# Kernel tuning notes

Measured on AMD Instinct MI355X. Metric: run time of the kernel, lower is better.

The kernel has to match this reference:

```python
import jax, jax.numpy as jnp
import numpy as np

C = jnp.complex64

def _ry_mat(t):
    c = jnp.cos(t / 2).astype(C)
    s = jnp.sin(t / 2).astype(C)
    return jnp.stack([jnp.stack([c, -s], -1), jnp.stack([s, c], -1)], -2)

def _rx_mat(t):
    c = jnp.cos(t / 2).astype(C)
    s = (-1j) * jnp.sin(t / 2).astype(C)
    return jnp.stack([jnp.stack([c, s], -1), jnp.stack([s, c], -1)], -2)

def _rz_mat(t):
    em = jnp.exp(-1j * (t / 2).astype(C))
    ep = jnp.exp(1j * (t / 2).astype(C))
    z = jnp.zeros_like(em)
    return jnp.stack([jnp.stack([em, z], -1), jnp.stack([z, ep], -1)], -2)

def _apply_1q(psi, gate, w):
    # psi: [bsz, 2^n]; gate: [2,2] (shared) or [bsz,2,2] (per-sample)
    bsz = psi.shape[0]
    s = psi.reshape(bsz, 1 << w, 2, -1)  # wire w isolated on axis 2
    if gate.ndim == 2:
        out = jnp.einsum('ij,bljr->blir', gate, s)
    else:
        out = jnp.einsum('bij,bljr->blir', gate, s)
    return out.reshape(bsz, -1)

def _apply_cnot(psi, c, t):
    bsz = psi.shape[0]
    a, b = min(c, t), max(c, t)
    s = psi.reshape(bsz, 1 << a, 2, 1 << (b - a - 1), 2, -1)
    if c < t:
        # control on axis 2, target on axis 4; after slicing ctrl=1, target -> axis 3
        s = s.at[:, :, 1].set(jnp.flip(s[:, :, 1], axis=3))
    else:
        # control on axis 4, target on axis 2
        s = s.at[:, :, :, :, 1].set(jnp.flip(s[:, :, :, :, 1], axis=2))
    return s.reshape(bsz, -1)

def setup_inputs() -> dict:
    key = jax.random.key(0)
    k1, k2 = jax.random.split(key)
    bsz, n_wires, n_qlayers = 1024, 14, 4
    x_raw = jax.random.normal(k1, (bsz, n_wires), dtype=jnp.float32)
    angles = jax.random.normal(k2, (n_qlayers, n_wires, 3), dtype=jnp.float32) * 0.1
    return {"x_raw": x_raw, "angles": angles}

def reference(x_raw, angles):
    L, n, _ = angles.shape
    bsz = x_raw.shape[0]
    x_enc = jnp.tanh(x_raw[:, :n]) * jnp.pi  # [bsz, n]
    # |0...0> statevector, wire 0 is the most significant bit
    psi = jnp.zeros((bsz, 1 << n), dtype=C).at[:, 0].set(1.0)
    # RY encoding (per-sample angles)
    for w in range(n):
        psi = _apply_1q(psi, _ry_mat(x_enc[:, w]), w)
    # variational layers
    for k in range(L):
        for w in range(n):
            psi = _apply_1q(psi, _rx_mat(angles[k, w, 0]), w)
            psi = _apply_1q(psi, _ry_mat(angles[k, w, 1]), w)
            psi = _apply_1q(psi, _rz_mat(angles[k, w, 2]), w)
        for i in range(n - 1):
            psi = _apply_cnot(psi, i, i + 1)
        psi = _apply_cnot(psi, n - 1, 0)
    # <Z_0>: +|amp|^2 when bit0=0, -|amp|^2 when bit0=1
    p = jnp.abs(psi.reshape(bsz, 2, -1)) ** 2
    return (p[:, 0].sum(-1) - p[:, 1].sum(-1)).astype(jnp.float32)
```

## Files before the change

kernel.cpp:

```cpp
#include <hip/hip_runtime.h>
#include <cmath>
#include <cstdint>

#define NW       14
#define NST      (1 << NW)
#define THREADS  512
#define PRETHR   768
#define NPASS    12
#define WTP      512

typedef _Float16 f16;
typedef _Float16 f16x8 __attribute__((ext_vector_type(8)));
typedef float    f32x4 __attribute__((ext_vector_type(4)));
typedef unsigned short u16;

struct PassArg { u16 Mm[4]; u16 Mt[3]; u16 Mw[3]; };
struct Plan { PassArg ps[NPASS]; u16 initM[14]; u16 measR; u16 _pad; };

__device__ __forceinline__ float2 cmulf(float2 a, float2 b) {
    return make_float2(a.x * b.x - a.y * b.y, a.x * b.y + a.y * b.x);
}
__device__ __host__ __forceinline__ unsigned wtofs(unsigned m, unsigned q01) {
    return (m * 16 + q01 * 8) ^ (((m >> 2) & 1u) << 3);
}

__global__ __launch_bounds__(PRETHR)
void vqc_pre(const float* __restrict__ angles, f16* __restrict__ wt_g,
             float2* __restrict__ u0_g)
{
    __shared__ float2 G[4 * NW * 4];
    const int tid = threadIdx.x;

    if (tid < 4 * NW) {
        const int k = tid / NW, w = tid % NW;
        const float a  = angles[(k * NW + w) * 3 + 0];
        const float bb = angles[(k * NW + w) * 3 + 1];
        const float c  = angles[(k * NW + w) * 3 + 2];
        float sa, ca, sb, cb, sc, cc;
        sincosf(a * 0.5f, &sa, &ca);
        sincosf(bb * 0.5f, &sb, &cb);
        sincosf(c * 0.5f, &sc, &cc);
        float2 m00 = make_float2(cb * ca,  sb * sa);
        float2 m01 = make_float2(-sb * ca, -cb * sa);
        float2 m10 = make_float2(sb * ca,  -cb * sa);
        float2 m11 = make_float2(cb * ca,  -sb * sa);
        const float2 e0 = make_float2(cc, -sc), e1 = make_float2(cc, sc);
        const float2 u00 = cmulf(e0, m00), u01 = cmulf(e0, m01);
        const float2 u10 = cmulf(e1, m10), u11 = cmulf(e1, m11);
        const int gi = (k * NW + w) * 4;
        G[gi + 0] = u00; G[gi + 1] = u01; G[gi + 2] = u10; G[gi + 3] = u11;
        if (k == 0) {
            u0_g[w * 4 + 0] = u00; u0_g[w * 4 + 1] = u01;
            u0_g[w * 4 + 2] = u10; u0_g[w * 4 + 3] = u11;
        }
    }
    __syncthreads();

    {
        const int p = tid >> 6, l6 = tid & 63;
        const int ap = l6 & 15, ahalf = (l6 >> 4) & 1, dup = l6 >> 5;
        const int layer = (p >> 2) + 1, g = p & 3;

        float2 p3;
        if (g == 3) {
            p3 = make_float2((((ap >> 3) & 1) == ahalf) ? 1.f : 0.f, 0.f);
        } else {
            const int wire = 13 - (10 - 4 * g + 3);
            p3 = G[(layer * NW + wire) * 4 + ((ap >> 3) & 1) * 2 + ahalf];
        }
        float2 e0a, e0b, e1a, e1b, e2a, e2b;
        {
            const int r0 = ap & 1, r1 = (ap >> 1) & 1, r2 = (ap >> 2) & 1;
            if (g == 3) {
                const float2* G13 = G + (layer * NW + 13) * 4;
                const float2* G12 = G + (layer * NW + 12) * 4;
                e0a = G13[r0 * 2 + 0]; e0b = G13[r0 * 2 + 1];
                e1a = G12[r1 * 2 + 0]; e1b = G12[r1 * 2 + 1];
                e2a = make_float2(r2 == 0 ? 1.f : 0.f, 0.f);
                e2b = make_float2(r2 == 1 ? 1.f : 0.f, 0.f);
            } else {
                const float2* G0 = G + (layer * NW + (13 - (10 - 4 * g + 0))) * 4;
                const float2* G1 = G + (layer * NW + (13 - (10 - 4 * g + 1))) * 4;
                const float2* G2 = G + (layer * NW + (13 - (10 - 4 * g + 2))) * 4;
                e0a = G0[r0 * 2 + 0]; e0b = G0[r0 * 2 + 1];
                e1a = G1[r1 * 2 + 0]; e1b = G1[r1 * 2 + 1];
                e2a = G2[r2 * 2 + 0]; e2b = G2[r2 * 2 + 1];
            }
        }
        f16x8 frag;
        #pragma unroll
        for (int j2 = 0; j2 < 8; ++j2) {
            float2 v = cmulf(p3, (j2 & 4) ? e2b : e2a);
            v = cmulf(v, (j2 & 2) ? e1b : e1a);
            v = cmulf(v, (j2 & 1) ? e0b : e0a);
            frag[j2] = (f16)(dup ? v.y : v.x);
        }
        *(f16x8*)(wt_g + p * WTP + dup * 256 + wtofs(ap, ahalf)) = frag;
    }
}

__global__ __launch_bounds__(THREADS, 4)
void vqc_kernel(const float* __restrict__ x_raw, const f16* __restrict__ wt_g,
                const float2* __restrict__ u0_g, float* __restrict__ out, Plan pl)
{
    extern __shared__ char smem[];
    f16*    Sh  = (f16*)smem;
    f16*    Wt  = Sh + 2 * NST;
    float2* G0c = (float2*)(Wt + NPASS * WTP);
    float*  red = (float*)(G0c + 2 * NW);

    const int b   = blockIdx.x;
    const int tid = threadIdx.x;
    const int lane = tid & 63, wv = tid >> 6;
    const int q = lane >> 4, m = lane & 15;

    {
        const uint4* src = (const uint4*)wt_g;
        uint4* dst = (uint4*)Wt;
        dst[tid] = src[tid];
        if (tid < 256) dst[512 + tid] = src[512 + tid];
    }
    if (tid < NW) {
        const float xe = tanhf(x_raw[b * NW + tid]) * 3.14159265358979f;
        float se, ce;
        sincosf(xe * 0.5f, &se, &ce);
        const float2 u00 = u0_g[tid * 4 + 0], u01 = u0_g[tid * 4 + 1];
        const float2 u10 = u0_g[tid * 4 + 2], u11 = u0_g[tid * 4 + 3];
        G0c[tid * 2 + 0] = make_float2(u00.x * ce + u01.x * se, u00.y * ce + u01.y * se);
        G0c[tid * 2 + 1] = make_float2(u10.x * ce + u11.x * se, u10.y * ce + u11.y * se);
    }
    __syncthreads();

    {
        float2 common = make_float2(1.f, 0.f);
        #pragma unroll
        for (int bit = 0; bit < 9; ++bit) {
            const int w = 13 - bit;
            const float2 f = ((tid >> bit) & 1) ? G0c[w * 2 + 1] : G0c[w * 2 + 0];
            common = cmulf(common, f);
        }
        unsigned p9 = 0;
        #pragma unroll
        for (int bit = 0; bit < 9; ++bit)
            p9 ^= ((tid >> bit) & 1) ? (unsigned)pl.initM[bit] : 0u;
        float2 f0[2], f1[2], f2[2], f3[2], f4[2];
        f0[0] = G0c[4*2+0]; f0[1] = G0c[4*2+1];
        f1[0] = G0c[3*2+0]; f1[1] = G0c[3*2+1];
        f2[0] = G0c[2*2+0]; f2[1] = G0c[2*2+1];
        f3[0] = G0c[1*2+0]; f3[1] = G0c[1*2+1];
        f4[0] = G0c[0*2+0]; f4[1] = G0c[0*2+1];
        #pragma unroll
        for (int j = 0; j < 32; ++j) {
            float2 o = cmulf(cmulf(f0[j & 1], f1[(j >> 1) & 1]),
                             cmulf(f2[(j >> 2) & 1], f3[(j >> 3) & 1]));
            o = cmulf(o, f4[(j >> 4) & 1]);
            const float2 amp = cmulf(common, o);
            const unsigned ph = p9
                ^ ((j & 1) ? pl.initM[9]  : 0) ^ ((j & 2)  ? pl.initM[10] : 0)
                ^ ((j & 4) ? pl.initM[11] : 0) ^ ((j & 8)  ? pl.initM[12] : 0)
                ^ ((j & 16) ? pl.initM[13] : 0);
            Sh[ph]       = (f16)amp.x;
            Sh[ph + NST] = (f16)amp.y;
        }
    }
    __syncthreads();

    const unsigned plane_off = (unsigned)(q >> 1) << 14;
    const unsigned q01 = (unsigned)(q & 1);
    const f32x4 z4 = {0.f, 0.f, 0.f, 0.f};
    #pragma unroll
    for (int p = 0; p < NPASS; ++p) {
        const PassArg& P = pl.ps[p];
        const unsigned pm = ((m & 1) ? P.Mm[0] : 0) ^ ((m & 2) ? P.Mm[1] : 0)
                          ^ ((m & 4) ? P.Mm[2] : 0) ^ ((m & 8) ? P.Mm[3] : 0);
        const unsigned wb = ((wv & 1) ? P.Mw[0] : 0) ^ ((wv & 2) ? P.Mw[1] : 0)
                          ^ ((wv & 4) ? P.Mw[2] : 0);
        const unsigned b0 = pm ^ wb;
        const f16x8 tr = *(const f16x8*)(Wt + p * WTP +       wtofs((unsigned)m, q01));
        const f16x8 ti = *(const f16x8*)(Wt + p * WTP + 256 + wtofs((unsigned)m, q01));
        const f16x8 bf1 = (q < 2) ? tr : -ti;
        const f16x8 bf2 = (q < 2) ? ti : tr;
        unsigned sw[8];
        f16x8 av[8];
        #pragma unroll
        for (int tt = 0; tt < 8; ++tt) {
            sw[tt] = b0 ^ ((tt & 1) ? P.Mt[0] : 0)
                        ^ ((tt & 2) ? P.Mt[1] : 0)
                        ^ ((tt & 4) ? P.Mt[2] : 0);
            av[tt] = *(const f16x8*)(Sh + plane_off + (sw[tt] ^ (q01 << 3)));
        }
        __syncthreads();
        #pragma unroll
        for (int tt = 0; tt < 8; ++tt) {
            const f32x4 d1 = __builtin_amdgcn_mfma_f32_16x16x32_f16(av[tt], bf1, z4, 0, 0, 0);
            const f32x4 d2 = __builtin_amdgcn_mfma_f32_16x16x32_f16(av[tt], bf2, z4, 0, 0, 0);
            union { f16 h[4]; uint2 u; } c1, c2;
            #pragma unroll
            for (int r = 0; r < 4; ++r) { c1.h[r] = (f16)d1[r]; c2.h[r] = (f16)d2[r]; }
            const unsigned wu = sw[tt] ^ ((unsigned)q << 2);
            *(uint2*)(Sh + wu)       = c1.u;
            *(uint2*)(Sh + NST + wu) = c2.u;
        }
        __syncthreads();
    }

    float acc = 0.f;
    {
        const unsigned base = (unsigned)tid * 32;
        const int pb = __popc(base & (unsigned)pl.measR) & 1;
        #pragma unroll
        for (int cch = 0; cch < 4; ++cch) {
            const unsigned co = (unsigned)cch * 8;
            const f16x8 rr = *(const f16x8*)(Sh + (base ^ co));
            const f16x8 ii = *(const f16x8*)(Sh + NST + (base ^ co));
            #pragma unroll
            for (int e = 0; e < 8; ++e) {
                const float re = (float)rr[e], im = (float)ii[e];
                const float pw = fmaf(re, re, im * im);
                const int sgn = pb ^ (__popc((co | (unsigned)e) & (unsigned)pl.measR) & 1);
                acc += sgn ? -pw : pw;
            }
        }
    }
    #pragma unroll
    for (int off = 32; off > 0; off >>= 1) acc += __shfl_down(acc, off);
    if ((tid & 63) == 0) red[wv] = acc;
    __syncthreads();
    if (tid == 0) {
        float s = 0.f;
        #pragma unroll
        for (int i = 0; i < THREADS / 64; ++i) s += red[i];
        out[b] = s;
    }
}

struct GFm { u16 col[14]; };

static unsigned ringp_host(unsigned x) {
    unsigned s = x;
    s ^= s >> 1; s ^= s >> 2; s ^= s >> 4; s ^= s >> 8;
    s &= 0x3FFFu;
    return (s ^ ((s & 1u) << 13)) & 0x3FFFu;
}
static u16 gf_apply(const GFm& m, u16 v) {
    u16 r = 0;
    for (int b = 0; b < 14; ++b) if ((v >> b) & 1) r ^= m.col[b];
    return r;
}
static GFm gf_compose(const GFm& A, const GFm& B) {
    GFm C;
    for (int b = 0; b < 14; ++b) C.col[b] = gf_apply(A, B.col[b]);
    return C;
}
static void rows_from(const GFm& A, u16 r[14]) {
    for (int i = 0; i < 14; ++i) {
        u16 mm = 0;
        for (int b = 0; b < 14; ++b) mm |= (u16)(((A.col[b] >> i) & 1) << b);
        r[i] = mm;
    }
}
static GFm from_rows(const u16 r[14]) {
    GFm A;
    for (int b = 0; b < 14; ++b) {
        u16 c = 0;
        for (int i = 0; i < 14; ++i) c |= (u16)(((r[i] >> b) & 1) << i);
        A.col[b] = c;
    }
    return A;
}
static GFm gf_inv(const GFm& A) {
    u16 M[14], I[14];
    rows_from(A, M);
    for (int i = 0; i < 14; ++i) I[i] = (u16)(1u << i);
    for (int c = 0; c < 14; ++c) {
        int p = c;
        while (p < 14 && !((M[p] >> c) & 1)) ++p;
        if (p == 14) continue;
        u16 t = M[c]; M[c] = M[p]; M[p] = t;
        t = I[c]; I[c] = I[p]; I[p] = t;
        for (int r2 = 0; r2 < 14; ++r2)
            if (r2 != c && ((M[r2] >> c) & 1)) { M[r2] ^= M[c]; I[r2] ^= I[c]; }
    }
    return from_rows(I);
}

static void build_plan(Plan& pl) {
    GFm ring, ringInv;
    for (int b = 0; b < 14; ++b) ring.col[b] = (u16)ringp_host(1u << b);
    ringInv = gf_inv(ring);

    GFm phi;
    for (int j = 0; j < 4; ++j) phi.col[10 + j] = (u16)(1u << j);
    for (int j = 0; j < 4; ++j) phi.col[6 + j]  = (u16)(1u << (4 + j));
    for (int j = 0; j < 4; ++j) phi.col[2 + j]  = (u16)(1u << (8 + j));
    phi.col[0] = (u16)(1u << 12);
    phi.col[1] = (u16)(1u << 13);

    for (int b = 0; b < 14; ++b) pl.initM[b] = gf_apply(phi, ring.col[b]);

    const int gb[4][4] = {{10,11,12,13},{6,7,8,9},{2,3,4,5},{0,1,6,7}};

    for (int p = 0; p < NPASS; ++p) {
        const int g = p & 3;
        u16 uv[4];
        if (g < 3) for (int j = 0; j < 4; ++j) uv[j] = (u16)(1u << gb[g + 1][j]);
        else       for (int j = 0; j < 4; ++j) uv[j] = ringInv.col[10 + j];
        for (int j = 0; j < 4; ++j) pl.ps[p].Mm[j] = gf_apply(phi, uv[j]);

        u16 span[14]; int ns = 0;
        u16 tv[6]; int nt = 0;
        auto tryAdd = [&](u16 v) -> bool {
            bool ch = true;
            while (ch) {
                ch = false;
                for (int i = 0; i < ns; ++i) {
                    const int tb = 31 - __builtin_clz((unsigned)span[i]);
                    if ((v >> tb) & 1) { v ^= span[i]; ch = true; }
                }
            }
            if (!v) return false;
            span[ns++] = v;
            return true;
        };
        for (int j = 0; j < 4; ++j) tryAdd((u16)(1u << gb[g][j]));
        for (int j = 0; j < 4; ++j) tryAdd(uv[j]);
        for (int b2 = 0; b2 < 14 && nt < 6; ++b2)
            if (tryAdd((u16)(1u << b2))) tv[nt++] = (u16)(1u << b2);
        for (int i = 0; i < 3; ++i) pl.ps[p].Mt[i] = gf_apply(phi, tv[i]);
        for (int i = 0; i < 3; ++i) pl.ps[p].Mw[i] = gf_apply(phi, tv[i + 3]);

        GFm Bm;
        for (int j = 0; j < 4; ++j) Bm.col[j]     = (u16)(1u << gb[g][j]);
        for (int j = 0; j < 4; ++j) Bm.col[4 + j] = uv[j];
        for (int i = 0; i < 6; ++i) Bm.col[8 + i] = tv[i];
        GFm Binv = gf_inv(Bm);
        u16 img[14];
        for (int j = 0; j < 4; ++j) img[j]     = pl.ps[p].Mm[j];
        for (int j = 0; j < 4; ++j) img[4 + j] = (u16)(1u << j);
        for (int i = 0; i < 6; ++i) img[8 + i] = gf_apply(phi, tv[i]);
        GFm nphi;
        for (int b2 = 0; b2 < 14; ++b2) {
            const u16 coef = gf_apply(Binv, (u16)(1u << b2));
            u16 v = 0;
            for (int j = 0; j < 14; ++j) if ((coef >> j) & 1) v ^= img[j];
            nphi.col[b2] = v;
        }
        if (g == 3) nphi = gf_compose(nphi, ringInv);
        phi = nphi;
    }

    GFm pinv = gf_inv(phi);
    u16 rows[14];
    rows_from(pinv, rows);
    pl.measR = rows[13];
    pl._pad = 0;
}

static u16 swz_h(u16 v) {
    return (u16)(v ^ ((((v >> 6) ^ (v >> 9) ^ (v >> 11)) & 7u) << 3));
}
static u16 swzT_h(u16 r) {
    u16 o = r;
    if ((r >> 3) & 1) o ^= (u16)((1u << 6) | (1u << 9)  | (1u << 11));
    if ((r >> 4) & 1) o ^= (u16)((1u << 7) | (1u << 10) | (1u << 12));
    if ((r >> 5) & 1) o ^= (u16)((1u << 8) | (1u << 11) | (1u << 13));
    return o;
}
static void fold_swzu(Plan& pl) {
    for (int p = 0; p < NPASS; ++p) {
        for (int j = 0; j < 4; ++j) pl.ps[p].Mm[j] = swz_h(pl.ps[p].Mm[j]);
        for (int j = 0; j < 3; ++j) pl.ps[p].Mt[j] = swz_h(pl.ps[p].Mt[j]);
        for (int j = 0; j < 3; ++j) pl.ps[p].Mw[j] = swz_h(pl.ps[p].Mw[j]);
    }
    for (int b = 0; b < 14; ++b) pl.initM[b] = swz_h(pl.initM[b]);
    pl.measR = swzT_h(pl.measR);
}

extern "C" void kernel_launch(void* const* d_in, const int* in_sizes, int n_in,
                              void* d_out, int out_size, void* d_ws, size_t ws_size,
                              hipStream_t stream) {
    const float* x_raw  = (const float*)d_in[0];
    const float* angles = (const float*)d_in[1];
    float* out = (float*)d_out;
    const int bsz = in_sizes[0] / NW;

    Plan pl;
    build_plan(pl);
    fold_swzu(pl);

    f16*    wt_g = (f16*)d_ws;
    float2* u0_g = (float2*)((char*)d_ws + (size_t)NPASS * WTP * sizeof(f16));

    vqc_pre<<<dim3(1), dim3(PRETHR), 0, stream>>>(angles, wt_g, u0_g);

    const size_t lds = (size_t)2 * NST * sizeof(f16)
                     + (size_t)NPASS * WTP * sizeof(f16)
                     + (size_t)(2 * NW) * sizeof(float2)
                     + (size_t)(THREADS / 64) * sizeof(float);
    (void)hipFuncSetAttribute((const void*)vqc_kernel,
                              hipFuncAttributeMaxDynamicSharedMemorySize, (int)lds);
    vqc_kernel<<<dim3(bsz), dim3(THREADS), lds, stream>>>(x_raw, wt_g, u0_g, out, pl);
}
```

Baseline: 111.5 us.

## Drop per-pass barrier, vectorize initial state writes, and linearize measurement reads

Removes the __syncthreads between the shared-memory loads and the in-place MFMA writes in each of the 12 passes. This relies on each wave reading and writing only its own addresses, so it saves a block-wide barrier per pass but races if that assumption fails. The product-state initialization is restructured as a shared product tree: each thread emits two 16-element runs as packed f16x8 stores instead of 32 scattered scalar stores. The final <Z0> reduction now reads contiguous, tid-strided chunks with parity computed per address, which should reduce LDS bank conflicts.

```diff
diff --git a/kernel.cpp b/kernel.cpp
--- a/kernel.cpp
+++ b/kernel.cpp
@@ -143,24 +143,59 @@
         #pragma unroll
         for (int bit = 0; bit < 9; ++bit)
             p9 ^= ((tid >> bit) & 1) ? (unsigned)pl.initM[bit] : 0u;
-        float2 f0[2], f1[2], f2[2], f3[2], f4[2];
-        f0[0] = G0c[4*2+0]; f0[1] = G0c[4*2+1];
-        f1[0] = G0c[3*2+0]; f1[1] = G0c[3*2+1];
-        f2[0] = G0c[2*2+0]; f2[1] = G0c[2*2+1];
-        f3[0] = G0c[1*2+0]; f3[1] = G0c[1*2+1];
-        f4[0] = G0c[0*2+0]; f4[1] = G0c[0*2+1];
-        #pragma unroll
-        for (int j = 0; j < 32; ++j) {
-            float2 o = cmulf(cmulf(f0[j & 1], f1[(j >> 1) & 1]),
-                             cmulf(f2[(j >> 2) & 1], f3[(j >> 3) & 1]));
-            o = cmulf(o, f4[(j >> 4) & 1]);
-            const float2 amp = cmulf(common, o);
-            const unsigned ph = p9
-                ^ ((j & 1) ? pl.initM[9]  : 0) ^ ((j & 2)  ? pl.initM[10] : 0)
-                ^ ((j & 4) ? pl.initM[11] : 0) ^ ((j & 8)  ? pl.initM[12] : 0)
-                ^ ((j & 16) ? pl.initM[13] : 0);
-            Sh[ph]       = (f16)amp.x;
-            Sh[ph + NST] = (f16)amp.y;
+
+        const float2 f0a = G0c[4*2+0], f0b = G0c[4*2+1];
+        const float2 f1a = G0c[3*2+0], f1b = G0c[3*2+1];
+        const float2 f2a = G0c[2*2+0], f2b = G0c[2*2+1];
+        const float2 f3a = G0c[1*2+0], f3b = G0c[1*2+1];
+        const float2 f4a = G0c[0*2+0], f4b = G0c[0*2+1];
+
+        const unsigned S   = (unsigned)pl.initM[13];
+        const unsigned Slo = S & 15u, Hh = S & ~15u;
+        const unsigned plo = p9 & 15u, B0 = p9 & ~15u;
+
+        #pragma unroll
+        for (int c = 0; c < 2; ++c) {
+            const unsigned r = plo ^ (c ? Slo : 0u);
+            const bool s0 = ((r       ) & 1u) != 0;
+            const bool s1 = (((r) ^ (r >> 1)) & 1u) != 0;
+            const bool s2 = (((r >> 1) ^ (r >> 2)) & 1u) != 0;
+            const bool s3 = (((r >> 2) ^ (r >> 3)) & 1u) != 0;
+            const bool s4 = ((((r >> 3) & 1u) ^ (unsigned)c) != 0);
+            const float2 F0[2] = { s0 ? f0b : f0a, s0 ? f0a : f0b };
+            const float2 F1[2] = { s1 ? f1b : f1a, s1 ? f1a : f1b };
+            const float2 F2[2] = { s2 ? f2b : f2a, s2 ? f2a : f2b };
+            const float2 F3[2] = { s3 ? f3b : f3a, s3 ? f3a : f3b };
+            const float2 F4[2] = { s4 ? f4b : f4a, s4 ? f4a : f4b };
+            const float2 A0 = cmulf(common, F4[0]);
+            const float2 A1 = cmulf(common, F4[1]);
+            float2 Bt[4];
+            Bt[0] = cmulf(A0, F3[0]); Bt[1] = cmulf(A0, F3[1]);
+            Bt[2] = cmulf(A1, F3[1]); Bt[3] = cmulf(A1, F3[0]);
+            float2 Ct[8];
+            #pragma unroll
+            for (int o32 = 0; o32 < 4; ++o32) {
+                const int o2 = o32 & 1;
+                Ct[o32 * 2 + 0] = cmulf(Bt[o32], F2[o2]);
+                Ct[o32 * 2 + 1] = cmulf(Bt[o32], F2[1 ^ o2]);
+            }
+            float2 Gt[4];
+            Gt[0] = cmulf(F1[0], F0[0]); Gt[1] = cmulf(F1[1], F0[1]);
+            Gt[2] = cmulf(F1[1], F0[0]); Gt[3] = cmulf(F1[0], F0[1]);
+
+            union { f16 h[8]; f16x8 v; } hR[2], hI[2];
+            #pragma unroll
+            for (int o = 0; o < 16; ++o) {
+                const int o0 = o & 1, o1 = (o >> 1) & 1;
+                const float2 amp = cmulf(Ct[o >> 1], Gt[o1 * 2 + o0]);
+                hR[o >> 3].h[o & 7] = (f16)amp.x;
+                hI[o >> 3].h[o & 7] = (f16)amp.y;
+            }
+            const unsigned bb = B0 ^ (c ? Hh : 0u);
+            *(f16x8*)(Sh + bb)           = hR[0].v;
+            *(f16x8*)(Sh + bb + 8)       = hR[1].v;
+            *(f16x8*)(Sh + NST + bb)     = hI[0].v;
+            *(f16x8*)(Sh + NST + bb + 8) = hI[1].v;
         }
     }
     __syncthreads();
@@ -189,7 +224,6 @@
                         ^ ((tt & 4) ? P.Mt[2] : 0);
             av[tt] = *(const f16x8*)(Sh + plane_off + (sw[tt] ^ (q01 << 3)));
         }
-        __syncthreads();
         #pragma unroll
         for (int tt = 0; tt < 8; ++tt) {
             const f32x4 d1 = __builtin_amdgcn_mfma_f32_16x16x32_f16(av[tt], bf1, z4, 0, 0, 0);
@@ -206,18 +240,17 @@
 
     float acc = 0.f;
     {
-        const unsigned base = (unsigned)tid * 32;
-        const int pb = __popc(base & (unsigned)pl.measR) & 1;
         #pragma unroll
         for (int cch = 0; cch < 4; ++cch) {
-            const unsigned co = (unsigned)cch * 8;
-            const f16x8 rr = *(const f16x8*)(Sh + (base ^ co));
-            const f16x8 ii = *(const f16x8*)(Sh + NST + (base ^ co));
+            const unsigned addr = (unsigned)cch * 4096u + (unsigned)tid * 8u;
+            const f16x8 rr = *(const f16x8*)(Sh + addr);
+            const f16x8 ii = *(const f16x8*)(Sh + NST + addr);
+            const int pb = __popc(addr & (unsigned)pl.measR) & 1;
             #pragma unroll
             for (int e = 0; e < 8; ++e) {
                 const float re = (float)rr[e], im = (float)ii[e];
                 const float pw = fmaf(re, re, im * im);
-                const int sgn = pb ^ (__popc((co | (unsigned)e) & (unsigned)pl.measR) & 1);
+                const int sgn = pb ^ (__popc((unsigned)e & (unsigned)pl.measR) & 1);
                 acc += sgn ? -pw : pw;
             }
         }
```

After: 108.1 us. 3.0% less time.
